# Performance work log

Hardware: AMD Instinct MI355X
Metric: run time of the kernel (lower is better)

## Reference

```python
import jax, jax.numpy as jnp
import numpy as np

L = 1024
D = 512      # d_model
H = 256      # hidden


def setup_inputs() -> dict:
    key = jax.random.key(0)
    k1, k2, k3, k4, k5 = jax.random.split(key, 5)
    scale = 0.02
    return {
        "seq_feats": jax.random.normal(k1, (L, D), dtype=jnp.float32),
        "W1": jax.random.normal(k2, (H, 2 * D), dtype=jnp.float32) * scale,
        "b1": jax.random.normal(k3, (H,), dtype=jnp.float32) * scale,
        "W2": jax.random.normal(k4, (1, H), dtype=jnp.float32) * scale,
        "b2": jax.random.normal(k5, (1,), dtype=jnp.float32) * scale,
    }


def reference(seq_feats, W1, b1, W2, b2):
    # cat([a, b]) @ W1.T == a @ W1[:, :D].T + b @ W1[:, D:].T
    # so we never materialize the [L, L, 2D] concat tensor.
    d = seq_feats.shape[1]
    pa = seq_feats @ W1[:, :d].T          # [L, H] (row / i contribution)
    pb = seq_feats @ W1[:, d:].T          # [L, H] (col / j contribution)
    h = jax.nn.relu(pa[:, None, :] + pb[None, :, :] + b1)  # [L, L, H]
    scores = jnp.einsum("ijh,h->ij", h, W2[0]) + b2[0]      # [L, L]
    scores = (scores + scores.T) * 0.5
    return jax.nn.sigmoid(scores)
```

## Files before the change

### kernel.cpp

```cpp
#include <hip/hip_runtime.h>
#include <math.h>

#define LL 1024
#define DD 512
#define HH 256


__global__ __launch_bounds__(512) void sp_gemm(
    const float* __restrict__ S, const float* __restrict__ W1,
    float* __restrict__ pC) {
  __shared__ float Sl[2][128][36];
  __shared__ float Wl[2][64][36];

  const int tid = threadIdx.x;
  const int tx  = tid & 15;
  const int ty  = tid >> 4;
  const int i0  = blockIdx.x * 128;
  const int n0  = blockIdx.y * 64;
  const int kz  = blockIdx.z * 128;

  const int srow = tid >> 3;
  const int ssl  = tid & 7;
  const int wn   = n0 + srow;
  const float* s0 = S + (size_t)(i0 + srow) * DD + kz + 4 * ssl;
  const float* s1 = S + (size_t)(i0 + 64 + srow) * DD + kz + 4 * ssl;
  const float* w0 = W1 + (size_t)(wn & 255) * (2 * DD) + (wn >> 8) * DD + kz + 4 * ssl;

  float4 sA, sB, wA;
  auto ld = [&](int c) {
    sA = *(const float4*)(s0 + 32 * c);
    sB = *(const float4*)(s1 + 32 * c);
    wA = *(const float4*)(w0 + 32 * c);
  };
  auto st = [&](int b) {
    *(float4*)&Sl[b][srow][4 * ssl]      = sA;
    *(float4*)&Sl[b][64 + srow][4 * ssl] = sB;
    *(float4*)&Wl[b][srow][4 * ssl]      = wA;
  };

  float acc[4][4] = {{0.f}};

  ld(0); st(0); __syncthreads();

  for (int c = 0; c < 4; ++c) {
    const int cur = c & 1;
    if (c < 3) ld(c + 1);
    #pragma unroll 2
    for (int k4 = 0; k4 < 8; ++k4) {
      float4 wf[4], sf[4];
      #pragma unroll
      for (int b = 0; b < 4; ++b) wf[b] = *(const float4*)&Wl[cur][tx + 16 * b][4 * k4];
      #pragma unroll
      for (int a = 0; a < 4; ++a) sf[a] = *(const float4*)&Sl[cur][4 * ty + a][4 * k4];
      #pragma unroll
      for (int a = 0; a < 4; ++a) {
        #pragma unroll
        for (int b = 0; b < 4; ++b) {
          acc[a][b] += sf[a].x * wf[b].x + sf[a].y * wf[b].y +
                       sf[a].z * wf[b].z + sf[a].w * wf[b].w;
        }
      }
    }
    if (c < 3) st(cur ^ 1);
    __syncthreads();
  }

  float* base = pC + (size_t)blockIdx.z * (512 * LL);
  #pragma unroll
  for (int b = 0; b < 4; ++b) {
    const int n = n0 + tx + 16 * b;
    *(float4*)(base + (size_t)n * LL + i0 + 4 * ty) =
        make_float4(acc[0][b], acc[1][b], acc[2][b], acc[3][b]);
  }
}

__global__ __launch_bounds__(256) void sp_pairwise(
    const float* __restrict__ pC, const float* __restrict__ b1,
    const float* __restrict__ W2, float* __restrict__ pz) {
  __shared__ float Tl[128][72];
  __shared__ float Ul[128][72];
  __shared__ float PR[2][128];
  __shared__ float As[64], Bs[64];

  const int tid = threadIdx.x;
  const int tx  = tid & 15;
  const int ty  = tid >> 4;
  const int j0  = blockIdx.x * 64;
  const int i0  = blockIdx.y * 64;
  const int hz  = blockIdx.z * 128;
  const size_t PZ = 512 * (size_t)LL;

  #pragma unroll 2
  for (int q = 0; q < 8; ++q) {
    const int m = q * 256 + tid;
    const int hh = m >> 4;
    const int g4 = (m & 15) * 4;
    const int h  = hz + hh;
    const float* pt = pC + (size_t)h * LL + i0 + g4;
    const float* pu = pC + (size_t)(HH + h) * LL + j0 + g4;
    const float4 t0 = *(const float4*)(pt);
    const float4 t1 = *(const float4*)(pt + PZ);
    const float4 t2 = *(const float4*)(pt + 2 * PZ);
    const float4 t3 = *(const float4*)(pt + 3 * PZ);
    const float4 u0 = *(const float4*)(pu);
    const float4 u1 = *(const float4*)(pu + PZ);
    const float4 u2 = *(const float4*)(pu + 2 * PZ);
    const float4 u3 = *(const float4*)(pu + 3 * PZ);
    const float bb = b1[h];
    *(float4*)&Tl[hh][g4] = make_float4(t0.x + t1.x + t2.x + t3.x + bb,
                                        t0.y + t1.y + t2.y + t3.y + bb,
                                        t0.z + t1.z + t2.z + t3.z + bb,
                                        t0.w + t1.w + t2.w + t3.w + bb);
    *(float4*)&Ul[hh][g4] = make_float4(u0.x + u1.x + u2.x + u3.x,
                                        u0.y + u1.y + u2.y + u3.y,
                                        u0.z + u1.z + u2.z + u3.z,
                                        u0.w + u1.w + u2.w + u3.w);
  }
  __syncthreads();

  {
    const int x = tid & 127, hs = tid >> 7;
    const float* pan = (x < 64) ? &Tl[0][x] : &Ul[0][x - 64];
    float p = 0.f;
    #pragma unroll 8
    for (int n = 0; n < 64; ++n) {
      const int hh = hs * 64 + n;
      p = fmaf(pan[hh * 72], W2[hz + hh], p);
    }
    PR[hs][x] = p;
  }
  __syncthreads();
  if (tid < 128) {
    const float s = PR[0][tid] + PR[1][tid];
    if (tid < 64) As[tid] = s; else Bs[tid - 64] = s;
  }
  __syncthreads();

  float acc[4][4] = {{0.f}};

  #pragma unroll 4
  for (int hh = 0; hh < 128; ++hh) {
    const float4 tv4 = *(const float4*)&Tl[hh][4 * ty];
    const float4 uv4 = *(const float4*)&Ul[hh][4 * tx];
    const float w = W2[hz + hh];
    const float tv[4] = {tv4.x, tv4.y, tv4.z, tv4.w};
    const float uv[4] = {uv4.x, uv4.y, uv4.z, uv4.w};
    #pragma unroll
    for (int a = 0; a < 4; ++a) {
      #pragma unroll
      for (int b = 0; b < 4; ++b) {
        acc[a][b] = fmaf(fabsf(tv[a] + uv[b]), w, acc[a][b]);
      }
    }
  }

  float* po = pz + (size_t)blockIdx.z * ((size_t)LL * LL);
  #pragma unroll
  for (int a = 0; a < 4; ++a) {
    const float Ai = As[4 * ty + a];
    float4 v;
    v.x = acc[a][0] + Ai + Bs[4 * tx + 0];
    v.y = acc[a][1] + Ai + Bs[4 * tx + 1];
    v.z = acc[a][2] + Ai + Bs[4 * tx + 2];
    v.w = acc[a][3] + Ai + Bs[4 * tx + 3];
    *(float4*)(po + (size_t)(i0 + 4 * ty + a) * LL + j0 + 4 * tx) = v;
  }
}

__global__ __launch_bounds__(1024) void sp_symsig(
    const float* __restrict__ pz, const float* __restrict__ b2,
    float* __restrict__ out) {
  const int bx = blockIdx.x, by = blockIdx.y;
  if (by > bx) return;
  __shared__ float B[64][65];
  __shared__ float O2[64][65];
  const int i0 = by * 64;
  const int j0 = bx * 64;
  const int r  = threadIdx.x >> 4;
  const int g  = threadIdx.x & 15;
  const size_t L2 = (size_t)LL * LL;

  const float* pm = pz + (size_t)(j0 + r) * LL + i0 + 4 * g;
  const float4 m0 = *(const float4*)(pm);
  const float4 m1 = *(const float4*)(pm + L2);
  B[r][4 * g + 0] = m0.x + m1.x;
  B[r][4 * g + 1] = m0.y + m1.y;
  B[r][4 * g + 2] = m0.z + m1.z;
  B[r][4 * g + 3] = m0.w + m1.w;
  __syncthreads();

  const float* pd = pz + (size_t)(i0 + r) * LL + j0 + 4 * g;
  const float4 d0 = *(const float4*)(pd);
  const float4 d1 = *(const float4*)(pd + L2);
  const float bb = b2[0];
  float4 o;
  float x;
  x = 0.25f * (d0.x + d1.x + B[4 * g + 0][r]) + bb; o.x = 1.f / (1.f + expf(-x));
  x = 0.25f * (d0.y + d1.y + B[4 * g + 1][r]) + bb; o.y = 1.f / (1.f + expf(-x));
  x = 0.25f * (d0.z + d1.z + B[4 * g + 2][r]) + bb; o.z = 1.f / (1.f + expf(-x));
  x = 0.25f * (d0.w + d1.w + B[4 * g + 3][r]) + bb; o.w = 1.f / (1.f + expf(-x));
  *(float4*)(out + (size_t)(i0 + r) * LL + j0 + 4 * g) = o;

  if (bx == by) return;

  O2[r][4 * g + 0] = o.x;
  O2[r][4 * g + 1] = o.y;
  O2[r][4 * g + 2] = o.z;
  O2[r][4 * g + 3] = o.w;
  __syncthreads();
  float4 t;
  t.x = O2[4 * g + 0][r];
  t.y = O2[4 * g + 1][r];
  t.z = O2[4 * g + 2][r];
  t.w = O2[4 * g + 3][r];
  *(float4*)(out + (size_t)(j0 + r) * LL + i0 + 4 * g) = t;
}

extern "C" void kernel_launch(void* const* d_in, const int* in_sizes, int n_in,
                              void* d_out, int out_size, void* d_ws, size_t ws_size,
                              hipStream_t stream) {
  const float* S  = (const float*)d_in[0];
  const float* W1 = (const float*)d_in[1];
  const float* b1 = (const float*)d_in[2];
  const float* W2 = (const float*)d_in[3];
  const float* b2 = (const float*)d_in[4];
  float* out = (float*)d_out;

  float* ws = (float*)d_ws;
  float* pC = ws;
  float* pz = ws + 4 * 512 * LL;

  hipLaunchKernelGGL(sp_gemm, dim3(8, 8, 4), dim3(512), 0, stream,
                     S, W1, pC);
  hipLaunchKernelGGL(sp_pairwise, dim3(16, 16, 2), dim3(256), 0, stream,
                     pC, b1, W2, pz);
  hipLaunchKernelGGL(sp_symsig, dim3(16, 16), dim3(1024), 0, stream,
                     pz, b2, out);
}
```

Before: 51.83 us.

## Reduce split-K partials once into bf16 buffer before pairwise stage

```diff
diff --git a/kernel.cpp b/kernel.cpp
--- a/kernel.cpp
+++ b/kernel.cpp
@@ -1,10 +1,18 @@
 #include <hip/hip_runtime.h>
+#include <hip/hip_bf16.h>
 #include <math.h>
 
 #define LL 1024
 #define DD 512
 #define HH 256
 
+
+__device__ __forceinline__ ushort f2bf(float f) {
+  __hip_bfloat16 h = __float2bfloat16(f);
+  return *reinterpret_cast<ushort*>(&h);
+}
+__device__ __forceinline__ float bf_lo(unsigned int u) { return __uint_as_float(u << 16); }
+__device__ __forceinline__ float bf_hi(unsigned int u) { return __uint_as_float(u & 0xffff0000u); }
 
 __global__ __launch_bounds__(512) void sp_gemm(
     const float* __restrict__ S, const float* __restrict__ W1,
@@ -74,11 +82,33 @@
   }
 }
 
-__global__ __launch_bounds__(256) void sp_pairwise(
+__global__ __launch_bounds__(256) void sp_reduce(
     const float* __restrict__ pC, const float* __restrict__ b1,
-    const float* __restrict__ W2, float* __restrict__ pz) {
-  __shared__ float Tl[128][72];
-  __shared__ float Ul[128][72];
+    ushort* __restrict__ O) {
+  const int m = blockIdx.x * 256 + threadIdx.x;
+  const int n = m >> 8;
+  const int NW = 512 * 256;
+  const float4* p = (const float4*)pC + m;
+  float4 a  = p[0];
+  const float4 v1 = p[NW], v2 = p[2 * NW], v3 = p[3 * NW];
+  a.x += v1.x + v2.x + v3.x;
+  a.y += v1.y + v2.y + v3.y;
+  a.z += v1.z + v2.z + v3.z;
+  a.w += v1.w + v2.w + v3.w;
+  if (n < 256) {
+    const float bb = b1[n];
+    a.x += bb; a.y += bb; a.z += bb; a.w += bb;
+  }
+  ushort4 o;
+  o.x = f2bf(a.x); o.y = f2bf(a.y); o.z = f2bf(a.z); o.w = f2bf(a.w);
+  *(ushort4*)(O + 4 * (size_t)m) = o;
+}
+
+__global__ __launch_bounds__(256, 4) void sp_pairwise(
+    const ushort* __restrict__ O, const float* __restrict__ W2,
+    float* __restrict__ pz) {
+  __shared__ ushort Tl[128][72];
+  __shared__ ushort Ul[128][72];
   __shared__ float PR[2][128];
   __shared__ float As[64], Bs[64];
 
@@ -88,44 +118,28 @@
   const int j0  = blockIdx.x * 64;
   const int i0  = blockIdx.y * 64;
   const int hz  = blockIdx.z * 128;
-  const size_t PZ = 512 * (size_t)LL;
-
-  #pragma unroll 2
+
+  #pragma unroll
   for (int q = 0; q < 8; ++q) {
     const int m = q * 256 + tid;
     const int hh = m >> 4;
-    const int g4 = (m & 15) * 4;
-    const int h  = hz + hh;
-    const float* pt = pC + (size_t)h * LL + i0 + g4;
-    const float* pu = pC + (size_t)(HH + h) * LL + j0 + g4;
-    const float4 t0 = *(const float4*)(pt);
-    const float4 t1 = *(const float4*)(pt + PZ);
-    const float4 t2 = *(const float4*)(pt + 2 * PZ);
-    const float4 t3 = *(const float4*)(pt + 3 * PZ);
-    const float4 u0 = *(const float4*)(pu);
-    const float4 u1 = *(const float4*)(pu + PZ);
-    const float4 u2 = *(const float4*)(pu + 2 * PZ);
-    const float4 u3 = *(const float4*)(pu + 3 * PZ);
-    const float bb = b1[h];
-    *(float4*)&Tl[hh][g4] = make_float4(t0.x + t1.x + t2.x + t3.x + bb,
-                                        t0.y + t1.y + t2.y + t3.y + bb,
-                                        t0.z + t1.z + t2.z + t3.z + bb,
-                                        t0.w + t1.w + t2.w + t3.w + bb);
-    *(float4*)&Ul[hh][g4] = make_float4(u0.x + u1.x + u2.x + u3.x,
-                                        u0.y + u1.y + u2.y + u3.y,
-                                        u0.z + u1.z + u2.z + u3.z,
-                                        u0.w + u1.w + u2.w + u3.w);
+    const int g8 = (m & 15) * 4;
+    *(ushort4*)&Tl[hh][g8] =
+        *(const ushort4*)(O + (size_t)(hz + hh) * LL + i0 + g8);
+    *(ushort4*)&Ul[hh][g8] =
+        *(const ushort4*)(O + (size_t)(HH + hz + hh) * LL + j0 + g8);
   }
   __syncthreads();
 
   {
     const int x = tid & 127, hs = tid >> 7;
-    const float* pan = (x < 64) ? &Tl[0][x] : &Ul[0][x - 64];
+    const ushort* pan = (x < 64) ? &Tl[0][x] : &Ul[0][x - 64];
     float p = 0.f;
     #pragma unroll 8
     for (int n = 0; n < 64; ++n) {
       const int hh = hs * 64 + n;
-      p = fmaf(pan[hh * 72], W2[hz + hh], p);
+      const float v = __uint_as_float(((unsigned int)pan[hh * 72]) << 16);
+      p = fmaf(v, W2[hz + hh], p);
     }
     PR[hs][x] = p;
   }
@@ -140,11 +154,11 @@
 
   #pragma unroll 4
   for (int hh = 0; hh < 128; ++hh) {
-    const float4 tv4 = *(const float4*)&Tl[hh][4 * ty];
-    const float4 uv4 = *(const float4*)&Ul[hh][4 * tx];
+    const uint2 tr = *(const uint2*)&Tl[hh][4 * ty];
+    const uint2 ur = *(const uint2*)&Ul[hh][4 * tx];
     const float w = W2[hz + hh];
-    const float tv[4] = {tv4.x, tv4.y, tv4.z, tv4.w};
-    const float uv[4] = {uv4.x, uv4.y, uv4.z, uv4.w};
+    const float tv[4] = {bf_lo(tr.x), bf_hi(tr.x), bf_lo(tr.y), bf_hi(tr.y)};
+    const float uv[4] = {bf_lo(ur.x), bf_hi(ur.x), bf_lo(ur.y), bf_hi(ur.y)};
     #pragma unroll
     for (int a = 0; a < 4; ++a) {
       #pragma unroll
@@ -170,12 +184,9 @@
 __global__ __launch_bounds__(1024) void sp_symsig(
     const float* __restrict__ pz, const float* __restrict__ b2,
     float* __restrict__ out) {
-  const int bx = blockIdx.x, by = blockIdx.y;
-  if (by > bx) return;
   __shared__ float B[64][65];
-  __shared__ float O2[64][65];
-  const int i0 = by * 64;
-  const int j0 = bx * 64;
+  const int i0 = blockIdx.y * 64;
+  const int j0 = blockIdx.x * 64;
   const int r  = threadIdx.x >> 4;
   const int g  = threadIdx.x & 15;
   const size_t L2 = (size_t)LL * LL;
@@ -200,20 +211,6 @@
   x = 0.25f * (d0.z + d1.z + B[4 * g + 2][r]) + bb; o.z = 1.f / (1.f + expf(-x));
   x = 0.25f * (d0.w + d1.w + B[4 * g + 3][r]) + bb; o.w = 1.f / (1.f + expf(-x));
   *(float4*)(out + (size_t)(i0 + r) * LL + j0 + 4 * g) = o;
-
-  if (bx == by) return;
-
-  O2[r][4 * g + 0] = o.x;
-  O2[r][4 * g + 1] = o.y;
-  O2[r][4 * g + 2] = o.z;
-  O2[r][4 * g + 3] = o.w;
-  __syncthreads();
-  float4 t;
-  t.x = O2[4 * g + 0][r];
-  t.y = O2[4 * g + 1][r];
-  t.z = O2[4 * g + 2][r];
-  t.w = O2[4 * g + 3][r];
-  *(float4*)(out + (size_t)(j0 + r) * LL + i0 + 4 * g) = t;
 }
 
 extern "C" void kernel_launch(void* const* d_in, const int* in_sizes, int n_in,
@@ -228,12 +225,15 @@
 
   float* ws = (float*)d_ws;
   float* pC = ws;
-  float* pz = ws + 4 * 512 * LL;
+  ushort* O = (ushort*)(ws + 4 * 512 * LL);
+  float* pz = ws + 4 * 512 * LL + 262144;
 
   hipLaunchKernelGGL(sp_gemm, dim3(8, 8, 4), dim3(512), 0, stream,
                      S, W1, pC);
+  hipLaunchKernelGGL(sp_reduce, dim3(512), dim3(256), 0, stream,
+                     pC, b1, O);
   hipLaunchKernelGGL(sp_pairwise, dim3(16, 16, 2), dim3(256), 0, stream,
-                     pC, b1, W2, pz);
+                     O, W2, pz);
   hipLaunchKernelGGL(sp_symsig, dim3(16, 16), dim3(1024), 0, stream,
                      pz, b2, out);
 }
```

Measured after the change: 50.11 us. 1.03x faster.
